# Performance work log

Hardware: AMD Instinct MI355X
Metric: run time of the kernel (lower is better)

The kernel has to match this reference:

```python
import jax, jax.numpy as jnp
import numpy as np

N = 50000        # nodes
E = 800000       # edges
F_IN = 32        # float features (x also carries 1 trailing cell-id column)
CELL_DIM = 16
NUM_CELLS = 854
C = 64           # out_channels
H0, H1 = 2, 1    # heads schedule for num_layers=2 -> [2, 1]
D_IN = F_IN + CELL_DIM  # 48, GAT input dim after cell embedding concat
NEG_SLOPE = 0.2  # PyG GATConv default negative_slope


def setup_inputs() -> dict:
    key = jax.random.key(0)
    ks = jax.random.split(key, 14)
    base = jax.random.normal(ks[0], (N, F_IN), jnp.float32)
    cell_ids = jax.random.randint(ks[1], (N,), 0, NUM_CELLS)
    x = jnp.concatenate([base, cell_ids.astype(jnp.float32)[:, None]], axis=1)
    edge_index = jax.random.randint(ks[2], (2, E), 0, N, dtype=jnp.int32)
    s = lambda f: 1.0 / np.sqrt(f)
    emb = jax.random.normal(ks[3], (NUM_CELLS, CELL_DIM), jnp.float32)
    W0 = jax.random.normal(ks[4], (D_IN, H0 * C), jnp.float32) * s(D_IN)
    a_src0 = jax.random.normal(ks[5], (H0, C), jnp.float32) * s(C)
    a_dst0 = jax.random.normal(ks[6], (H0, C), jnp.float32) * s(C)
    b0 = jnp.zeros((C,), jnp.float32)
    ln_g = jnp.ones((C,), jnp.float32)
    ln_b = jnp.zeros((C,), jnp.float32)
    W1 = jax.random.normal(ks[7], (C, H1 * C), jnp.float32) * s(C)
    a_src1 = jax.random.normal(ks[8], (H1, C), jnp.float32) * s(C)
    a_dst1 = jax.random.normal(ks[9], (H1, C), jnp.float32) * s(C)
    b1 = jnp.zeros((C,), jnp.float32)
    return {"x": x, "edge_index": edge_index, "emb": emb,
            "W0": W0, "a_src0": a_src0, "a_dst0": a_dst0, "b0": b0,
            "ln_g": ln_g, "ln_b": ln_b,
            "W1": W1, "a_src1": a_src1, "a_dst1": a_dst1, "b1": b1}


def gat_layer(h_in, src, dst, W, a_src, a_dst, b, heads):
    # h_in: [N, D]; src/dst: [E'] (self-loops already appended)
    h = (h_in @ W).reshape(N, heads, C)                 # [N, H, C]
    alpha_s = jnp.einsum('nhc,hc->nh', h, a_src)        # [N, H]
    alpha_d = jnp.einsum('nhc,hc->nh', h, a_dst)
    e = jax.nn.leaky_relu(alpha_s[src] + alpha_d[dst], NEG_SLOPE)  # [E', H]
    # segment softmax over incoming edges of each dst node
    m = jax.ops.segment_max(e, dst, num_segments=N)     # [N, H]
    ex = jnp.exp(e - m[dst])
    denom = jax.ops.segment_sum(ex, dst, num_segments=N)
    alpha = ex / denom[dst]                             # [E', H]
    msg = h[src] * alpha[:, :, None]                    # [E', H, C]
    out = jax.ops.segment_sum(msg, dst, num_segments=N) # [N, H, C]
    return out.mean(axis=1) + b                         # concat=False -> mean over heads


def layer_norm(x, g, b):
    mu = x.mean(-1, keepdims=True)
    var = ((x - mu) ** 2).mean(-1, keepdims=True)
    return (x - mu) * jax.lax.rsqrt(var + 1e-5) * g + b


def reference(x, edge_index, emb, W0, a_src0, a_dst0, b0, ln_g, ln_b,
              W1, a_src1, a_dst1, b1):
    base = x[:, :-1]
    cell_ids = x[:, -1].astype(jnp.int32)
    h = jnp.concatenate([base, emb[cell_ids]], axis=1)  # [N, 48]
    # add self-loops (PyG GATConv default add_self_loops=True)
    loop = jnp.arange(N, dtype=edge_index.dtype)
    src = jnp.concatenate([edge_index[0], loop])
    dst = jnp.concatenate([edge_index[1], loop])
    h = gat_layer(h, src, dst, W0, a_src0, a_dst0, b0, H0)
    h = jax.nn.elu(layer_norm(h, ln_g, ln_b))           # dropout is identity at eval
    h = gat_layer(h, src, dst, W1, a_src1, a_dst1, b1, H1)
    return h
```

## Files before the change

### kernel.cpp

```cpp
#include <hip/hip_runtime.h>
#include <hip/hip_bf16.h>

#define N_NODES 50000
#define N_EDGES 800000
#define E_TOT 850000
#define F_IN 32
#define CELL_DIM 16
#define D_IN 48
#define X_STRIDE 33
#define NUM_CELLS 854
#define NEG_SLOPE 0.2f
#define SCAN_BLOCKS 49
#define NODE0_BLOCKS 2048
#define HIST_BLOCKS 3125

typedef unsigned int uint;
typedef unsigned short ushort;

static __device__ __forceinline__ uint f2b(float f) {
  uint x = __float_as_uint(f);
  return (x + 0x7fffu + ((x >> 16) & 1u)) >> 16;
}
static __device__ __forceinline__ float b2f_lo(uint w) { return __uint_as_float(w << 16); }
static __device__ __forceinline__ float b2f_hi(uint w) { return __uint_as_float(w & 0xffff0000u); }
static __device__ __forceinline__ float lrelu(float e) { return e > 0.f ? e : NEG_SLOPE * e; }


__global__ __launch_bounds__(256, 4) void k_node0h(const float* __restrict__ x,
                                                   const float* __restrict__ emb,
                                                   const float* __restrict__ W0,
                                                   const float* __restrict__ asrc,
                                                   const float* __restrict__ adst,
                                                   const int* __restrict__ ei,
                                                   uint* __restrict__ h0p,
                                                   float2* __restrict__ as0,
                                                   float2* __restrict__ ad0,
                                                   int* __restrict__ deg) {
  int tid = threadIdx.x;
  if (blockIdx.x >= NODE0_BLOCKS) {
    int e = (blockIdx.x - NODE0_BLOCKS) * 256 + tid;
    if (e < N_EDGES) atomicAdd(&deg[ei[N_EDGES + e]], 1);
    return;
  }
  __shared__ float hin_s[4][4][48];
  int lane = tid & 63, wid = tid >> 6;
  float2 w0r[D_IN];
#pragma unroll
  for (int k = 0; k < D_IN; ++k)
    w0r[k] = make_float2(W0[k * 128 + lane], W0[k * 128 + 64 + lane]);
  float a_s0 = asrc[lane], a_s1 = asrc[64 + lane];
  float a_d0 = adst[lane], a_d1 = adst[64 + lane];

  int gw = blockIdx.x * 4 + wid;
  for (int g = gw; g < N_NODES / 4; g += NODE0_BLOCKS * 4) {
    int nb = g * 4;
#pragma unroll
    for (int j = 0; j < 4; ++j) {
      int n = nb + j;
      float t = 0.f;
      if (lane < 33) t = x[n * X_STRIDE + lane];
      int cid = (int)__shfl(t, 32, 64);
      cid = cid < 0 ? 0 : (cid >= NUM_CELLS ? NUM_CELLS - 1 : cid);
      if (lane >= 32 && lane < 48) t = emb[cid * CELL_DIM + (lane - 32)];
      if (lane < 48) hin_s[wid][j][lane] = t;
    }
#pragma unroll
    for (int j = 0; j < 4; ++j) {
      int n = nb + j;
      const float4* hp = (const float4*)hin_s[wid][j];
      float acc0 = 0.f, acc1 = 0.f;
#pragma unroll
      for (int k4 = 0; k4 < 12; ++k4) {
        float4 h = hp[k4];
        acc0 = fmaf(h.x, w0r[4 * k4 + 0].x, acc0); acc1 = fmaf(h.x, w0r[4 * k4 + 0].y, acc1);
        acc0 = fmaf(h.y, w0r[4 * k4 + 1].x, acc0); acc1 = fmaf(h.y, w0r[4 * k4 + 1].y, acc1);
        acc0 = fmaf(h.z, w0r[4 * k4 + 2].x, acc0); acc1 = fmaf(h.z, w0r[4 * k4 + 2].y, acc1);
        acc0 = fmaf(h.w, w0r[4 * k4 + 3].x, acc0); acc1 = fmaf(h.w, w0r[4 * k4 + 3].y, acc1);
      }
      h0p[n * 64 + lane] = f2b(acc0) | (f2b(acc1) << 16);
      float sa0 = acc0 * a_s0, sa1 = acc1 * a_s1;
      float sd0 = acc0 * a_d0, sd1 = acc1 * a_d1;
#pragma unroll
      for (int o = 32; o >= 1; o >>= 1) {
        sa0 += __shfl_xor(sa0, o, 64);
        sa1 += __shfl_xor(sa1, o, 64);
        sd0 += __shfl_xor(sd0, o, 64);
        sd1 += __shfl_xor(sd1, o, 64);
      }
      if (lane == 0) {
        as0[n] = make_float2(sa0, sa1);
        ad0[n] = make_float2(sd0, sd1);
      }
    }
  }
}


__global__ __launch_bounds__(1024) void k_scan1(const int* __restrict__ deg, int* __restrict__ off,
                                                int* __restrict__ bsum) {
  __shared__ int ws[16];
  int tid = threadIdx.x;
  int lane = tid & 63, wid = tid >> 6;
  int i = blockIdx.x * 1024 + tid;
  int v = (i < N_NODES) ? deg[i] + 1 : 0;
  int sc = v;
#pragma unroll
  for (int o = 1; o < 64; o <<= 1) {
    int t = __shfl_up(sc, o, 64);
    if (lane >= o) sc += t;
  }
  if (lane == 63) ws[wid] = sc;
  __syncthreads();
  if (tid < 16) {
    int w = ws[tid];
    int s = w;
#pragma unroll
    for (int o = 1; o < 16; o <<= 1) {
      int t = __shfl_up(s, o, 64);
      if (tid >= o) s += t;
    }
    ws[tid] = s - w;
  }
  __syncthreads();
  int excl = sc - v + ws[wid];
  if (i < N_NODES) off[i] = excl;
  if (tid == 1023) bsum[blockIdx.x] = excl + v;
}

__global__ __launch_bounds__(1024) void k_scan23(int* __restrict__ off, int* __restrict__ ofs,
                                                 const int* __restrict__ bsum) {
  __shared__ int carry_s;
  int tid = threadIdx.x;
  if (tid < 64) {
    int v = (tid < SCAN_BLOCKS) ? bsum[tid] : 0;
    int s = v;
#pragma unroll
    for (int o = 1; o < 64; o <<= 1) {
      int t = __shfl_up(s, o, 64);
      if (tid >= o) s += t;
    }
    if (tid == (int)blockIdx.x) carry_s = s - v;
  }
  __syncthreads();
  int carry = carry_s;
  int i = blockIdx.x * 1024 + tid;
  if (i < N_NODES) {
    int v = off[i] + carry;
    off[i] = v;
    ofs[i] = v;
  }
  if (i == 0) off[N_NODES] = E_TOT;
}

__global__ __launch_bounds__(256) void k_scatter(const int* __restrict__ ei, int* __restrict__ ofs,
                                                 const int* __restrict__ off,
                                                 const float2* __restrict__ as0v,
                                                 const float2* __restrict__ ad0v,
                                                 uint2* __restrict__ ew) {
  int t = blockIdx.x * 256 + threadIdx.x;
  if (t < N_EDGES) {
    int s = ei[t], d = ei[N_EDGES + t];
    float2 a_s = as0v[s], a_d = ad0v[d];
    float w0 = __expf(lrelu(a_s.x + a_d.x));
    float w1 = __expf(lrelu(a_s.y + a_d.y));
    int p = atomicAdd(&ofs[d], 1);
    ew[p] = make_uint2((uint)s, f2b(w0) | (f2b(w1) << 16));
  } else if (t < N_EDGES + N_NODES) {
    int n = t - N_EDGES;
    int slot = off[n + 1] - 1;
    float2 a_s = as0v[n], a_d = ad0v[n];
    float w0 = __expf(lrelu(a_s.x + a_d.x));
    float w1 = __expf(lrelu(a_s.y + a_d.y));
    ew[slot] = make_uint2((uint)n, f2b(w0) | (f2b(w1) << 16));
  }
}


__global__ __launch_bounds__(256) void k_agg0(const int* __restrict__ off,
                                              const uint2* __restrict__ ew,
                                              const uint* __restrict__ h0p,
                                              const float* __restrict__ b0,
                                              const float* __restrict__ lng,
                                              const float* __restrict__ lnb,
                                              const float* __restrict__ W1,
                                              const float* __restrict__ asrc1,
                                              const float* __restrict__ adst1,
                                              ushort* __restrict__ h1b,
                                              float* __restrict__ as1, float* __restrict__ ad1) {
  int n = blockIdx.x * 4 + (threadIdx.x >> 6);
  int lane = threadIdx.x & 63;
  float acc0 = 0.f, acc1 = 0.f, den0 = 0.f, den1 = 0.f;
  int i0 = off[n], i1 = off[n + 1];
  int i = i0;
  for (; i + 7 < i1; i += 8) {
    uint2 r[8];
    uint h[8];
#pragma unroll
    for (int j = 0; j < 8; ++j) r[j] = ew[i + j];
#pragma unroll
    for (int j = 0; j < 8; ++j) h[j] = h0p[r[j].x * 64 + lane];
#pragma unroll
    for (int j = 0; j < 8; ++j) {
      float w;
      w = b2f_lo(r[j].y); acc0 += w * b2f_lo(h[j]); den0 += w;
      w = b2f_hi(r[j].y); acc1 += w * b2f_hi(h[j]); den1 += w;
    }
  }
  for (; i + 3 < i1; i += 4) {
    uint2 r[4];
    uint h[4];
#pragma unroll
    for (int j = 0; j < 4; ++j) r[j] = ew[i + j];
#pragma unroll
    for (int j = 0; j < 4; ++j) h[j] = h0p[r[j].x * 64 + lane];
#pragma unroll
    for (int j = 0; j < 4; ++j) {
      float w;
      w = b2f_lo(r[j].y); acc0 += w * b2f_lo(h[j]); den0 += w;
      w = b2f_hi(r[j].y); acc1 += w * b2f_hi(h[j]); den1 += w;
    }
  }
  for (; i < i1; ++i) {
    uint2 r = ew[i];
    uint h = h0p[r.x * 64 + lane];
    float w;
    w = b2f_lo(r.y); acc0 += w * b2f_lo(h); den0 += w;
    w = b2f_hi(r.y); acc1 += w * b2f_hi(h); den1 += w;
  }
  float v = 0.5f * (acc0 / den0 + acc1 / den1) + b0[lane];
  float mu = v;
#pragma unroll
  for (int o = 32; o >= 1; o >>= 1) mu += __shfl_xor(mu, o, 64);
  mu *= (1.0f / 64.0f);
  float d = v - mu;
  float vr = d * d;
#pragma unroll
  for (int o = 32; o >= 1; o >>= 1) vr += __shfl_xor(vr, o, 64);
  vr *= (1.0f / 64.0f);
  float y = d * rsqrtf(vr + 1e-5f) * lng[lane] + lnb[lane];
  y = y > 0.f ? y : expm1f(y);
  float h1v = 0.f;
#pragma unroll
  for (int k = 0; k < 64; ++k) {
    float yk = __shfl(y, k, 64);
    h1v += yk * W1[k * 64 + lane];
  }
  h1b[n * 64 + lane] = (ushort)f2b(h1v);
  float sa = h1v * asrc1[lane];
  float sdv = h1v * adst1[lane];
#pragma unroll
  for (int o = 32; o >= 1; o >>= 1) {
    sa += __shfl_xor(sa, o, 64);
    sdv += __shfl_xor(sdv, o, 64);
  }
  if (lane == 0) {
    as1[n] = sa;
    ad1[n] = sdv;
  }
}


__global__ __launch_bounds__(256) void k_agg1(const int* __restrict__ off,
                                              const uint2* __restrict__ ew,
                                              const ushort* __restrict__ h1b,
                                              const float* __restrict__ as1,
                                              const float* __restrict__ ad1,
                                              const float* __restrict__ b1,
                                              float* __restrict__ out) {
  int n = blockIdx.x * 4 + (threadIdx.x >> 6);
  int lane = threadIdx.x & 63;
  float adv = ad1[n];
  float acc = 0.f, den = 0.f;
  int i0 = off[n], i1 = off[n + 1];
  int i = i0;
  for (; i + 7 < i1; i += 8) {
    uint s[8];
    float a[8];
    uint h[8];
#pragma unroll
    for (int j = 0; j < 8; ++j) s[j] = ew[i + j].x;
#pragma unroll
    for (int j = 0; j < 8; ++j) a[j] = as1[s[j]];
#pragma unroll
    for (int j = 0; j < 8; ++j) h[j] = h1b[s[j] * 64 + lane];
#pragma unroll
    for (int j = 0; j < 8; ++j) {
      float w = __expf(lrelu(a[j] + adv));
      acc += w * __uint_as_float(h[j] << 16);
      den += w;
    }
  }
  for (; i + 3 < i1; i += 4) {
    uint s[4];
    float a[4];
    uint h[4];
#pragma unroll
    for (int j = 0; j < 4; ++j) s[j] = ew[i + j].x;
#pragma unroll
    for (int j = 0; j < 4; ++j) a[j] = as1[s[j]];
#pragma unroll
    for (int j = 0; j < 4; ++j) h[j] = h1b[s[j] * 64 + lane];
#pragma unroll
    for (int j = 0; j < 4; ++j) {
      float w = __expf(lrelu(a[j] + adv));
      acc += w * __uint_as_float(h[j] << 16);
      den += w;
    }
  }
  for (; i < i1; ++i) {
    uint s = ew[i].x;
    float w = __expf(lrelu(as1[s] + adv));
    acc += w * __uint_as_float((uint)h1b[s * 64 + lane] << 16);
    den += w;
  }
  out[n * 64 + lane] = acc / den + b1[lane];
}


extern "C" void kernel_launch(void* const* d_in, const int* in_sizes, int n_in,
                              void* d_out, int out_size, void* d_ws, size_t ws_size,
                              hipStream_t stream) {
  const float* x    = (const float*)d_in[0];
  const int*   ei   = (const int*)d_in[1];
  const float* emb  = (const float*)d_in[2];
  const float* W0   = (const float*)d_in[3];
  const float* as0w = (const float*)d_in[4];
  const float* ad0w = (const float*)d_in[5];
  const float* b0   = (const float*)d_in[6];
  const float* lng  = (const float*)d_in[7];
  const float* lnb  = (const float*)d_in[8];
  const float* W1   = (const float*)d_in[9];
  const float* as1w = (const float*)d_in[10];
  const float* ad1w = (const float*)d_in[11];
  const float* b1   = (const float*)d_in[12];
  float* out = (float*)d_out;

  uint2* ew  = (uint2*)d_ws;
  float* as0 = (float*)(ew + E_TOT);
  float* ad0 = as0 + N_NODES * 2;
  float* as1 = ad0 + N_NODES * 2;
  float* ad1 = as1 + N_NODES;
  uint* h0p = (uint*)(ad1 + N_NODES);
  ushort* h1b = (ushort*)(h0p + N_NODES * 64);
  int* deg  = (int*)(h1b + N_NODES * 64);
  int* off  = deg + N_NODES;
  int* ofs  = off + N_NODES + 1;
  int* bsum = ofs + N_NODES;

  hipMemsetAsync(deg, 0, N_NODES * sizeof(int), stream);
  k_node0h<<<NODE0_BLOCKS + HIST_BLOCKS, 256, 0, stream>>>(x, emb, W0, as0w, ad0w, ei, h0p,
                                                           (float2*)as0, (float2*)ad0, deg);
  k_scan1<<<SCAN_BLOCKS, 1024, 0, stream>>>(deg, off, bsum);
  k_scan23<<<SCAN_BLOCKS, 1024, 0, stream>>>(off, ofs, bsum);
  k_scatter<<<(N_EDGES + N_NODES + 255) / 256, 256, 0, stream>>>(ei, ofs, off, (const float2*)as0,
                                                                 (const float2*)ad0, ew);
  k_agg0<<<N_NODES / 4, 256, 0, stream>>>(off, ew, h0p, b0, lng, lnb, W1, as1w, ad1w,
                                          h1b, as1, ad1);
  k_agg1<<<N_NODES / 4, 256, 0, stream>>>(off, ew, h1b, as1, ad1, b1, out);
}
```

Measured before the change: 280.1 us.

## Split node projection heads across waves to halve weight registers per thread

The first-layer node projection now assigns one head per wave instead of both heads per lane. Each thread holds 48 weight floats instead of 96, and the block shares an 8-node input tile through LDS with __syncthreads. The aim is to reduce register pressure and raise occupancy. In exchange it adds block barriers, 16-bit interleaved stores instead of packed 32-bit stores, and separate scalar attention writes per head.

```diff
diff --git a/kernel.cpp b/kernel.cpp
--- a/kernel.cpp
+++ b/kernel.cpp
@@ -26,72 +26,71 @@
 static __device__ __forceinline__ float lrelu(float e) { return e > 0.f ? e : NEG_SLOPE * e; }
 
 
-__global__ __launch_bounds__(256, 4) void k_node0h(const float* __restrict__ x,
-                                                   const float* __restrict__ emb,
-                                                   const float* __restrict__ W0,
-                                                   const float* __restrict__ asrc,
-                                                   const float* __restrict__ adst,
-                                                   const int* __restrict__ ei,
-                                                   uint* __restrict__ h0p,
-                                                   float2* __restrict__ as0,
-                                                   float2* __restrict__ ad0,
-                                                   int* __restrict__ deg) {
+__global__ __launch_bounds__(256) void k_node0h(const float* __restrict__ x,
+                                                const float* __restrict__ emb,
+                                                const float* __restrict__ W0,
+                                                const float* __restrict__ asrc,
+                                                const float* __restrict__ adst,
+                                                const int* __restrict__ ei,
+                                                ushort* __restrict__ h0u,
+                                                float* __restrict__ as0, float* __restrict__ ad0,
+                                                int* __restrict__ deg) {
   int tid = threadIdx.x;
   if (blockIdx.x >= NODE0_BLOCKS) {
     int e = (blockIdx.x - NODE0_BLOCKS) * 256 + tid;
     if (e < N_EDGES) atomicAdd(&deg[ei[N_EDGES + e]], 1);
     return;
   }
-  __shared__ float hin_s[4][4][48];
+  __shared__ float hin[8][48];
   int lane = tid & 63, wid = tid >> 6;
-  float2 w0r[D_IN];
-#pragma unroll
-  for (int k = 0; k < D_IN; ++k)
-    w0r[k] = make_float2(W0[k * 128 + lane], W0[k * 128 + 64 + lane]);
-  float a_s0 = asrc[lane], a_s1 = asrc[64 + lane];
-  float a_d0 = adst[lane], a_d1 = adst[64 + lane];
-
-  int gw = blockIdx.x * 4 + wid;
-  for (int g = gw; g < N_NODES / 4; g += NODE0_BLOCKS * 4) {
-    int nb = g * 4;
-#pragma unroll
-    for (int j = 0; j < 4; ++j) {
-      int n = nb + j;
+  int h = wid & 1;
+  int q = wid >> 1;
+  float w0r[D_IN];
+#pragma unroll
+  for (int k = 0; k < D_IN; ++k) w0r[k] = W0[k * 128 + h * 64 + lane];
+  float av_s = asrc[h * 64 + lane], av_d = adst[h * 64 + lane];
+
+  for (int g = blockIdx.x; g < N_NODES / 8; g += NODE0_BLOCKS) {
+    int nb = g * 8;
+#pragma unroll
+    for (int j = 0; j < 2; ++j) {
+      int loc = 2 * wid + j;
+      int n = nb + loc;
       float t = 0.f;
       if (lane < 33) t = x[n * X_STRIDE + lane];
       int cid = (int)__shfl(t, 32, 64);
       cid = cid < 0 ? 0 : (cid >= NUM_CELLS ? NUM_CELLS - 1 : cid);
       if (lane >= 32 && lane < 48) t = emb[cid * CELL_DIM + (lane - 32)];
-      if (lane < 48) hin_s[wid][j][lane] = t;
-    }
+      if (lane < 48) hin[loc][lane] = t;
+    }
+    __syncthreads();
 #pragma unroll
     for (int j = 0; j < 4; ++j) {
-      int n = nb + j;
-      const float4* hp = (const float4*)hin_s[wid][j];
-      float acc0 = 0.f, acc1 = 0.f;
+      int loc = 4 * q + j;
+      int n = nb + loc;
+      const float4* hp = (const float4*)hin[loc];
+      float acc = 0.f;
 #pragma unroll
       for (int k4 = 0; k4 < 12; ++k4) {
-        float4 h = hp[k4];
-        acc0 = fmaf(h.x, w0r[4 * k4 + 0].x, acc0); acc1 = fmaf(h.x, w0r[4 * k4 + 0].y, acc1);
-        acc0 = fmaf(h.y, w0r[4 * k4 + 1].x, acc0); acc1 = fmaf(h.y, w0r[4 * k4 + 1].y, acc1);
-        acc0 = fmaf(h.z, w0r[4 * k4 + 2].x, acc0); acc1 = fmaf(h.z, w0r[4 * k4 + 2].y, acc1);
-        acc0 = fmaf(h.w, w0r[4 * k4 + 3].x, acc0); acc1 = fmaf(h.w, w0r[4 * k4 + 3].y, acc1);
+        float4 hh = hp[k4];
+        acc = fmaf(hh.x, w0r[4 * k4 + 0], acc);
+        acc = fmaf(hh.y, w0r[4 * k4 + 1], acc);
+        acc = fmaf(hh.z, w0r[4 * k4 + 2], acc);
+        acc = fmaf(hh.w, w0r[4 * k4 + 3], acc);
       }
-      h0p[n * 64 + lane] = f2b(acc0) | (f2b(acc1) << 16);
-      float sa0 = acc0 * a_s0, sa1 = acc1 * a_s1;
-      float sd0 = acc0 * a_d0, sd1 = acc1 * a_d1;
+      h0u[(n * 64 + lane) * 2 + h] = (ushort)f2b(acc);
+      float sa = acc * av_s, sd = acc * av_d;
 #pragma unroll
       for (int o = 32; o >= 1; o >>= 1) {
-        sa0 += __shfl_xor(sa0, o, 64);
-        sa1 += __shfl_xor(sa1, o, 64);
-        sd0 += __shfl_xor(sd0, o, 64);
-        sd1 += __shfl_xor(sd1, o, 64);
+        sa += __shfl_xor(sa, o, 64);
+        sd += __shfl_xor(sd, o, 64);
       }
       if (lane == 0) {
-        as0[n] = make_float2(sa0, sa1);
-        ad0[n] = make_float2(sd0, sd1);
+        as0[n * 2 + h] = sa;
+        ad0[n * 2 + h] = sd;
       }
     }
+    __syncthreads();
   }
 }
 
@@ -348,8 +347,8 @@
   int* bsum = ofs + N_NODES;
 
   hipMemsetAsync(deg, 0, N_NODES * sizeof(int), stream);
-  k_node0h<<<NODE0_BLOCKS + HIST_BLOCKS, 256, 0, stream>>>(x, emb, W0, as0w, ad0w, ei, h0p,
-                                                           (float2*)as0, (float2*)ad0, deg);
+  k_node0h<<<NODE0_BLOCKS + HIST_BLOCKS, 256, 0, stream>>>(x, emb, W0, as0w, ad0w, ei,
+                                                           (ushort*)h0p, as0, ad0, deg);
   k_scan1<<<SCAN_BLOCKS, 1024, 0, stream>>>(deg, off, bsum);
   k_scan23<<<SCAN_BLOCKS, 1024, 0, stream>>>(off, ofs, bsum);
   k_scatter<<<(N_EDGES + N_NODES + 255) / 256, 256, 0, stream>>>(ei, ofs, off, (const float2*)as0,
```

Result: no change. 278.4 us (-0.6%).
